# Kernel optimization log

Measured on AMD Instinct MI355X. Metric: run time of the kernel, lower is better.

The kernel has to match this reference:

```python
import jax, jax.numpy as jnp
import numpy as np


def setup_inputs() -> dict:
    key = jax.random.key(0)
    k1, k2 = jax.random.split(key)
    B, L = 16384, 4096
    # probabilities kept strictly inside (0,1) so log terms are finite
    p = jax.random.uniform(k1, (B, L), dtype=jnp.float32) * 0.98 + 0.01
    target = jax.random.randint(k2, (B, L), 0, 2, dtype=jnp.int32)
    return {"output_sigmoid": p, "target": target}


def reference(output_sigmoid, target):
    # per-element: -log(1-p) where target==0 else -log(p); mean over all elements
    logp = jnp.where(target == 0,
                     jnp.log1p(-output_sigmoid),
                     jnp.log(output_sigmoid))
    return -jnp.mean(logp)
```

## Files before the change

kernel.cpp:

```cpp
#include <hip/hip_runtime.h>
#include <hip/hip_bf16.h>


#define BLOCKS 2048
#define THREADS 256

__global__ __launch_bounds__(THREADS) void bce_partial_kernel(
    const float* __restrict__ p, const int* __restrict__ t,
    double* __restrict__ partial, long long nvec, long long n) {
  long long tid = (long long)blockIdx.x * blockDim.x + threadIdx.x;
  long long stride = (long long)gridDim.x * blockDim.x;

  float sum = 0.0f;
  const float4* p4 = reinterpret_cast<const float4*>(p);
  const int4* t4 = reinterpret_cast<const int4*>(t);
  for (long long i = tid; i < nvec; i += stride) {
    float4 pv = p4[i];
    int4 tv = t4[i];
    sum += __logf(tv.x ? pv.x : 1.0f - pv.x);
    sum += __logf(tv.y ? pv.y : 1.0f - pv.y);
    sum += __logf(tv.z ? pv.z : 1.0f - pv.z);
    sum += __logf(tv.w ? pv.w : 1.0f - pv.w);
  }
  long long tail_start = nvec * 4;
  long long tail_n = n - tail_start;
  if (tid < tail_n) {
    long long i = tail_start + tid;
    sum += __logf(t[i] ? p[i] : 1.0f - p[i]);
  }

  for (int off = 32; off > 0; off >>= 1) sum += __shfl_down(sum, off);

  __shared__ float wsum[THREADS / 64];
  int lane = threadIdx.x & 63;
  int wave = threadIdx.x >> 6;
  if (lane == 0) wsum[wave] = sum;
  __syncthreads();
  if (threadIdx.x == 0) {
    double bsum = 0.0;
    #pragma unroll
    for (int w = 0; w < THREADS / 64; ++w) bsum += (double)wsum[w];
    partial[blockIdx.x] = bsum;
  }
}

__global__ __launch_bounds__(256) void bce_final_kernel(
    const double* __restrict__ partial, int nparts, float* __restrict__ out,
    double inv_n) {
  double s = 0.0;
  for (int i = threadIdx.x; i < nparts; i += blockDim.x) s += partial[i];
  for (int off = 32; off > 0; off >>= 1) s += __shfl_down(s, off);
  __shared__ double wsum[4];
  int lane = threadIdx.x & 63;
  int wave = threadIdx.x >> 6;
  if (lane == 0) wsum[wave] = s;
  __syncthreads();
  if (threadIdx.x == 0) {
    double tot = wsum[0] + wsum[1] + wsum[2] + wsum[3];
    out[0] = (float)(-tot * inv_n);
  }
}

extern "C" void kernel_launch(void* const* d_in, const int* in_sizes, int n_in,
                              void* d_out, int out_size, void* d_ws, size_t ws_size,
                              hipStream_t stream) {
  const float* p = (const float*)d_in[0];
  const int* t = (const int*)d_in[1];
  float* out = (float*)d_out;
  double* partial = (double*)d_ws;

  long long n = (long long)in_sizes[0];
  long long nvec = n / 4;

  long long want = (nvec + THREADS - 1) / THREADS;
  int blocks = (int)(want < BLOCKS ? (want > 0 ? want : 1) : BLOCKS);

  bce_partial_kernel<<<blocks, THREADS, 0, stream>>>(p, t, partial, nvec, n);
  bce_final_kernel<<<1, 256, 0, stream>>>(partial, blocks, out, 1.0 / (double)n);
}
```

Before: 504.7 us.

## Add size-specialized BCE kernel with batched nontemporal loads and log2 math

Result: no change. 498.4 us (-1.2%).

```diff
diff --git a/kernel.cpp b/kernel.cpp
--- a/kernel.cpp
+++ b/kernel.cpp
@@ -4,33 +4,33 @@
 
 #define BLOCKS 2048
 #define THREADS 256
+#define NELEM 67108864LL
+#define NVEC 16777216LL
+#define STRIDE_VEC 524288
+#define OUTER 8
 
-__global__ __launch_bounds__(THREADS) void bce_partial_kernel(
-    const float* __restrict__ p, const int* __restrict__ t,
-    double* __restrict__ partial, long long nvec, long long n) {
-  long long tid = (long long)blockIdx.x * blockDim.x + threadIdx.x;
-  long long stride = (long long)gridDim.x * blockDim.x;
+typedef float  f32x4 __attribute__((ext_vector_type(4)));
+typedef int    i32x4 __attribute__((ext_vector_type(4)));
 
-  float sum = 0.0f;
-  const float4* p4 = reinterpret_cast<const float4*>(p);
-  const int4* t4 = reinterpret_cast<const int4*>(t);
-  for (long long i = tid; i < nvec; i += stride) {
-    float4 pv = p4[i];
-    int4 tv = t4[i];
-    sum += __logf(tv.x ? pv.x : 1.0f - pv.x);
-    sum += __logf(tv.y ? pv.y : 1.0f - pv.y);
-    sum += __logf(tv.z ? pv.z : 1.0f - pv.z);
-    sum += __logf(tv.w ? pv.w : 1.0f - pv.w);
-  }
-  long long tail_start = nvec * 4;
-  long long tail_n = n - tail_start;
-  if (tid < tail_n) {
-    long long i = tail_start + tid;
-    sum += __logf(t[i] ? p[i] : 1.0f - p[i]);
-  }
+__device__ __forceinline__ float lg2(float x) {
+#if __has_builtin(__builtin_amdgcn_logf)
+  return __builtin_amdgcn_logf(x);
+#else
+  return __log2f(x);
+#endif
+}
 
+__device__ __forceinline__ float bce4_lg2(f32x4 pv, i32x4 tv) {
+  float a0 = tv.x ? pv.x : 1.0f - pv.x;
+  float a1 = tv.y ? pv.y : 1.0f - pv.y;
+  float a2 = tv.z ? pv.z : 1.0f - pv.z;
+  float a3 = tv.w ? pv.w : 1.0f - pv.w;
+  return (lg2(a0) + lg2(a1)) + (lg2(a2) + lg2(a3));
+}
+
+__device__ __forceinline__ void block_reduce_store(
+    float sum, double* __restrict__ partial) {
   for (int off = 32; off > 0; off >>= 1) sum += __shfl_down(sum, off);
-
   __shared__ float wsum[THREADS / 64];
   int lane = threadIdx.x & 63;
   int wave = threadIdx.x >> 6;
@@ -44,9 +44,54 @@
   }
 }
 
+__global__ __launch_bounds__(THREADS, 1) void bce_fast_kernel(
+    const float* __restrict__ p, const int* __restrict__ t,
+    double* __restrict__ partial) {
+  const char* pb = (const char*)p;
+  const char* tb = (const char*)t;
+  unsigned off = ((unsigned)(blockIdx.x * THREADS + threadIdx.x)) * 16u;
+  const unsigned SS = (unsigned)STRIDE_VEC * 16u;
+  float s0 = 0.0f, s1 = 0.0f, s2 = 0.0f, s3 = 0.0f;
+  #pragma unroll 2
+  for (int o = 0; o < OUTER; ++o) {
+    f32x4 pa = __builtin_nontemporal_load((const f32x4*)(pb + off));
+    f32x4 pb_ = __builtin_nontemporal_load((const f32x4*)(pb + off + SS));
+    f32x4 pc = __builtin_nontemporal_load((const f32x4*)(pb + off + 2 * SS));
+    f32x4 pd = __builtin_nontemporal_load((const f32x4*)(pb + off + 3 * SS));
+    i32x4 ta = __builtin_nontemporal_load((const i32x4*)(tb + off));
+    i32x4 tb_ = __builtin_nontemporal_load((const i32x4*)(tb + off + SS));
+    i32x4 tc = __builtin_nontemporal_load((const i32x4*)(tb + off + 2 * SS));
+    i32x4 td = __builtin_nontemporal_load((const i32x4*)(tb + off + 3 * SS));
+    s0 += bce4_lg2(pa, ta);
+    s1 += bce4_lg2(pb_, tb_);
+    s2 += bce4_lg2(pc, tc);
+    s3 += bce4_lg2(pd, td);
+    off += 4u * SS;
+  }
+  block_reduce_store((s0 + s1) + (s2 + s3), partial);
+}
+
+__global__ __launch_bounds__(THREADS) void bce_generic_kernel(
+    const float* __restrict__ p, const int* __restrict__ t,
+    double* __restrict__ partial, long long nvec, long long n) {
+  long long tid = (long long)blockIdx.x * blockDim.x + threadIdx.x;
+  long long stride = (long long)gridDim.x * blockDim.x;
+  const f32x4* p4 = reinterpret_cast<const f32x4*>(p);
+  const i32x4* t4 = reinterpret_cast<const i32x4*>(t);
+  float sum = 0.0f;
+  for (long long i = tid; i < nvec; i += stride)
+    sum += bce4_lg2(p4[i], t4[i]);
+  long long tail_start = nvec * 4;
+  if (tid < n - tail_start) {
+    long long j = tail_start + tid;
+    sum += lg2(t[j] ? p[j] : 1.0f - p[j]);
+  }
+  block_reduce_store(sum, partial);
+}
+
 __global__ __launch_bounds__(256) void bce_final_kernel(
     const double* __restrict__ partial, int nparts, float* __restrict__ out,
-    double inv_n) {
+    double scale) {
   double s = 0.0;
   for (int i = threadIdx.x; i < nparts; i += blockDim.x) s += partial[i];
   for (int off = 32; off > 0; off >>= 1) s += __shfl_down(s, off);
@@ -57,7 +102,7 @@
   __syncthreads();
   if (threadIdx.x == 0) {
     double tot = wsum[0] + wsum[1] + wsum[2] + wsum[3];
-    out[0] = (float)(-tot * inv_n);
+    out[0] = (float)(-tot * scale);
   }
 }
 
@@ -70,11 +115,16 @@
   double* partial = (double*)d_ws;
 
   long long n = (long long)in_sizes[0];
-  long long nvec = n / 4;
+  const double LN2 = 0.69314718055994530942;
 
-  long long want = (nvec + THREADS - 1) / THREADS;
-  int blocks = (int)(want < BLOCKS ? (want > 0 ? want : 1) : BLOCKS);
-
-  bce_partial_kernel<<<blocks, THREADS, 0, stream>>>(p, t, partial, nvec, n);
-  bce_final_kernel<<<1, 256, 0, stream>>>(partial, blocks, out, 1.0 / (double)n);
+  if (n == NELEM) {
+    bce_fast_kernel<<<BLOCKS, THREADS, 0, stream>>>(p, t, partial);
+    bce_final_kernel<<<1, 256, 0, stream>>>(partial, BLOCKS, out, LN2 / (double)n);
+  } else {
+    long long nvec = n / 4;
+    long long want = (nvec + THREADS - 1) / THREADS;
+    int blocks = (int)(want < BLOCKS ? (want > 0 ? want : 1) : BLOCKS);
+    bce_generic_kernel<<<blocks, THREADS, 0, stream>>>(p, t, partial, nvec, n);
+    bce_final_kernel<<<1, 256, 0, stream>>>(partial, blocks, out, LN2 / (double)n);
+  }
 }
```
